# Kernel optimization log

Measured on AMD Instinct MI355X. Metric: run time of the kernel, lower is better.

The kernel has to match this reference:

```python
import jax, jax.numpy as jnp
import numpy as np
import math

B, N, D = 128, 50, 256      # batch, segments per piece, cross-attn feature dim
H_CA = 8                    # cross-attention heads
FP, H_AP = 64, 8            # pooling feature dim / heads
S = N * N                   # flattened similarity length (<= 2560 pos-enc cap)
TEMP = 1.0
LN_EPS = 1e-5


def _ln(x, g, b):
    mu = jnp.mean(x, -1, keepdims=True)
    var = jnp.mean((x - mu) ** 2, -1, keepdims=True)
    return (x - mu) * jax.lax.rsqrt(var + LN_EPS) * g + b


def setup_inputs() -> dict:
    key = jax.random.key(0)
    ks = jax.random.split(key, 32)
    w = lambda i, shp, s=0.02: jax.random.normal(ks[i], shp, jnp.float32) * s
    z = lambda shp: jnp.zeros(shp, jnp.float32)
    o = lambda shp: jnp.ones(shp, jnp.float32)
    return {
        "features1": jax.random.normal(ks[0], (B, N, D), jnp.float32),
        "features2": jax.random.normal(ks[1], (B, N, D), jnp.float32),
        # CrossAttention (weights stored (in,out) so x @ W + b)
        "ca_wq": w(2, (D, D)), "ca_bq": z((D,)),
        "ca_wk": w(3, (D, D)), "ca_bk": z((D,)),
        "ca_wv": w(4, (D, D)), "ca_bv": z((D,)),
        "ca_wo": w(5, (D, D)), "ca_bo": z((D,)),
        "ca_ln1_g": o((D,)), "ca_ln1_b": z((D,)),
        "ca_ln2_g": o((D,)), "ca_ln2_b": z((D,)),
        "ca_w1": w(6, (D, 2 * D)), "ca_b1": z((2 * D,)),
        "ca_w2": w(7, (2 * D, D)), "ca_b2": z((D,)),
        # LearnableMetricSimilarity
        "ms_metric": jnp.eye(D, dtype=jnp.float32),
        "ms_wt": w(8, (D, D)), "ms_bt": z((D,)),
        # AttentionPooling
        "ap_wq": w(9, (1, FP)), "ap_bq": z((FP,)),
        "ap_wk": w(10, (1, FP)), "ap_bk": z((FP,)),
        "ap_wv": w(11, (1, FP)), "ap_bv": z((FP,)),
        "ap_pos": w(12, (1, 2560, FP), 0.02),
        "ap_wo": w(13, (FP, FP)), "ap_bo": z((FP,)),
        "ap_ln_g": o((FP,)), "ap_ln_b": z((FP,)),
    }


def reference(features1, features2,
              ca_wq, ca_bq, ca_wk, ca_bk, ca_wv, ca_bv, ca_wo, ca_bo,
              ca_ln1_g, ca_ln1_b, ca_ln2_g, ca_ln2_b,
              ca_w1, ca_b1, ca_w2, ca_b2,
              ms_metric, ms_wt, ms_bt,
              ap_wq, ap_bq, ap_wk, ap_bk, ap_wv, ap_bv,
              ap_pos, ap_wo, ap_bo, ap_ln_g, ap_ln_b):
    hd = D // H_CA

    def attend(fx, fy):
        q = (fx @ ca_wq + ca_bq).reshape(B, N, H_CA, hd)
        k = (fy @ ca_wk + ca_bk).reshape(B, N, H_CA, hd)
        v = (fy @ ca_wv + ca_bv).reshape(B, N, H_CA, hd)
        # Faithful to original: tensors stay (B,N,H,hd), so matmul with
        # k.transpose(-2,-1) yields per-position head-vs-head attention (B,N,H,H).
        scores = jnp.einsum('bnhd,bngd->bnhg', q, k) / math.sqrt(hd)
        wts = jax.nn.softmax(scores, axis=-1)  # dropout is identity (eval)
        att = jnp.einsum('bnhg,bngd->bnhd', wts, v).reshape(B, N, D)
        x = _ln(fx + att @ ca_wo + ca_bo, ca_ln1_g, ca_ln1_b)
        ffn = jax.nn.relu(x @ ca_w1 + ca_b1) @ ca_w2 + ca_b2
        return _ln(x + ffn, ca_ln2_g, ca_ln2_b)

    e1 = attend(features1, features2)
    e2 = attend(features2, features1)

    # Learnable metric similarity: Mahalanobis distance via quadratic expansion
    # d_ij = t1_i M t1_i + t2_j M t2_j - 2 t1_i M t2_j  (M symmetrized)
    t1 = e1 @ ms_wt + ms_bt
    t2 = e2 @ ms_wt + ms_bt
    M = (ms_metric + ms_metric.T) * 0.5
    t1M = t1 @ M
    t2M = t2 @ M
    q1 = jnp.sum(t1M * t1, axis=-1)                    # (B,N)
    q2 = jnp.sum(t2M * t2, axis=-1)                    # (B,N)
    cross = jnp.einsum('bnd,bmd->bnm', t1M, t2)        # (B,N,N)
    dist = q1[:, :, None] + q2[:, None, :] - 2.0 * cross
    sim = jnp.exp(jnp.clip(-dist / TEMP, -10.0, 10.0))  # (B,N,N)

    # Attention pooling over flattened similarity matrix
    flat = sim.reshape(B, S, 1)
    pos = ap_pos[:, :S, :]
    hdp = FP // H_AP
    q = (flat @ ap_wq + ap_bq + pos).reshape(B, S, H_AP, hdp)
    k = (flat @ ap_wk + ap_bk + pos).reshape(B, S, H_AP, hdp)
    v = (flat @ ap_wv + ap_bv).reshape(B, S, H_AP, hdp)
    scores = jnp.einsum('bshd,bsgd->bshg', q, k) / math.sqrt(hdp)  # (B,S,H,H)
    wts = jax.nn.softmax(scores, axis=-1)
    att = jnp.einsum('bshg,bsgd->bshd', wts, v).reshape(B, S, FP)
    pooled = jnp.mean(att, axis=1) @ ap_wo + ap_bo     # (B,FP)
    return _ln(pooled, ap_ln_g, ap_ln_b)
```

## Files before the change

kernel.cpp:

```cpp
#include <hip/hip_runtime.h>
#include <cstddef>
#include <cstdint>


namespace esn {

constexpr int kB   = 128;
constexpr int kN   = 50;
constexpr int kR   = kB * kN;
constexpr int kR2  = 2 * kR;
constexpr int kS   = kN * kN;
constexpr int kChunks = 79;

typedef __attribute__((ext_vector_type(8))) short short8;
typedef __attribute__((ext_vector_type(4))) float f32x4;

__device__ inline ushort f2bf_rn(float v) {
  uint32_t u = __float_as_uint(v);
  uint32_t r = (u + 0x7fffu + ((u >> 16) & 1u)) >> 16;
  return (ushort)r;
}
__device__ inline float bf2f(ushort b) {
  return __uint_as_float(((uint32_t)b) << 16);
}
__device__ inline void split2(float v, ushort& h, ushort& l) {
  h = f2bf_rn(v);
  l = f2bf_rn(v - bf2f(h));
}

__device__ __forceinline__ void gld16(const ushort* g, ushort* l) {
  __builtin_amdgcn_global_load_lds(
      (const __attribute__((address_space(1))) void*)g,
      (__attribute__((address_space(3))) void*)l,
      16, 0, 0);
}

template<bool RELU, bool WF32, bool WSPLIT>
__global__ __launch_bounds__(256)
void gemm_mfma_kernel(const ushort* __restrict__ Ah, const ushort* __restrict__ Al, int lda,
                      const ushort* __restrict__ Bh, const ushort* __restrict__ Bl, int ldb,
                      const float* __restrict__ bias,
                      float* __restrict__ C, int ldc,
                      ushort* __restrict__ Ch, ushort* __restrict__ Cl,
                      int K)
{
  __shared__ __align__(16) ushort sAh[128 * 32];
  __shared__ __align__(16) ushort sAl[128 * 32];
  __shared__ __align__(16) ushort sBh[128 * 32];
  __shared__ __align__(16) ushort sBl[128 * 32];

  const int tid  = threadIdx.x;
  const int lane = tid & 63;
  const int wave = tid >> 6;
  const int wm   = wave >> 1, wn = wave & 1;
  const int bm   = blockIdx.x * 128, bn = blockIdx.y * 128;

  const int lrow  = lane >> 2;
  const int lslot = lane & 3;

  f32x4 acc[4][4] = {};

  const int nK = K >> 5;
  for (int kt = 0; kt < nK; kt++) {
    const int kk = kt << 5;
#pragma unroll
    for (int i = 0; i < 2; i++) {
      const int grp  = wave * 32 + i * 16;
      const int row  = grp + lrow;
      const int c    = lslot ^ ((row >> 1) & 3);
      const size_t aoff = (size_t)(bm + row) * lda + kk + c * 8;
      const size_t boff = (size_t)(bn + row) * ldb + kk + c * 8;
      gld16(Ah + aoff, sAh + grp * 32);
      gld16(Al + aoff, sAl + grp * 32);
      gld16(Bh + boff, sBh + grp * 32);
      gld16(Bl + boff, sBl + grp * 32);
    }
    __syncthreads();

    const int r16 = lane & 15, kq = lane >> 4;
    short8 afh[4], afl[4], bfh[4], bfl[4];
#pragma unroll
    for (int f = 0; f < 4; f++) {
      int arow = wm * 64 + f * 16 + r16;
      int sa = kq ^ ((arow >> 1) & 3);
      afh[f] = *(const short8*)(sAh + arow * 32 + sa * 8);
      afl[f] = *(const short8*)(sAl + arow * 32 + sa * 8);
      int brow = wn * 64 + f * 16 + r16;
      int sb = kq ^ ((brow >> 1) & 3);
      bfh[f] = *(const short8*)(sBh + brow * 32 + sb * 8);
      bfl[f] = *(const short8*)(sBl + brow * 32 + sb * 8);
    }
#pragma unroll
    for (int mf = 0; mf < 4; mf++)
#pragma unroll
      for (int nf = 0; nf < 4; nf++) {
        acc[mf][nf] = __builtin_amdgcn_mfma_f32_16x16x32_bf16(afh[mf], bfh[nf], acc[mf][nf], 0, 0, 0);
        acc[mf][nf] = __builtin_amdgcn_mfma_f32_16x16x32_bf16(afh[mf], bfl[nf], acc[mf][nf], 0, 0, 0);
        acc[mf][nf] = __builtin_amdgcn_mfma_f32_16x16x32_bf16(afl[mf], bfh[nf], acc[mf][nf], 0, 0, 0);
      }
    __syncthreads();
  }

  const int r16 = lane & 15, rq = lane >> 4;
#pragma unroll
  for (int nf = 0; nf < 4; nf++) {
    int col = bn + wn * 64 + nf * 16 + r16;
    float bv = bias ? bias[col] : 0.0f;
#pragma unroll
    for (int mf = 0; mf < 4; mf++) {
      int rowb = bm + wm * 64 + mf * 16 + rq * 4;
#pragma unroll
      for (int r = 0; r < 4; r++) {
        float v = acc[mf][nf][r] + bv;
        if (RELU) v = fmaxf(v, 0.0f);
        size_t off = (size_t)(rowb + r) * ldc + col;
        if (WF32) C[off] = v;
        if (WSPLIT) {
          ushort h, l; split2(v, h, l);
          Ch[off] = h; Cl[off] = l;
        }
      }
    }
  }
}

__global__ void prep_w_kernel(const float* __restrict__ wq, const float* __restrict__ wk,
                              const float* __restrict__ wv, const float* __restrict__ bq,
                              const float* __restrict__ bk, const float* __restrict__ bv,
                              const float* __restrict__ wo, const float* __restrict__ w1,
                              const float* __restrict__ w2, const float* __restrict__ wt,
                              const float* __restrict__ msm,
                              ushort* __restrict__ qkvh, ushort* __restrict__ qkvl,
                              ushort* __restrict__ woh,  ushort* __restrict__ wol,
                              ushort* __restrict__ w1h,  ushort* __restrict__ w1l,
                              ushort* __restrict__ w2h,  ushort* __restrict__ w2l,
                              ushort* __restrict__ wth,  ushort* __restrict__ wtl,
                              ushort* __restrict__ msh,  ushort* __restrict__ msl,
                              float* __restrict__ bqkv)
{
  int idx = blockIdx.x * 256 + threadIdx.x;
  if (idx < 768)
    bqkv[idx] = idx < 256 ? bq[idx] : idx < 512 ? bk[idx - 256] : bv[idx - 512];
  float v; ushort *oh, *ol; int off;
  if (idx < 196608) {
    int n = idx >> 8, k = idx & 255;
    v = n < 256 ? wq[k * 256 + n] : n < 512 ? wk[k * 256 + n - 256] : wv[k * 256 + n - 512];
    oh = qkvh; ol = qkvl; off = idx;
  } else if (idx < 262144) {
    int i = idx - 196608; int n = i >> 8, k = i & 255;
    v = wo[k * 256 + n]; oh = woh; ol = wol; off = i;
  } else if (idx < 393216) {
    int i = idx - 262144; int n = i >> 8, k = i & 255;
    v = w1[k * 512 + n]; oh = w1h; ol = w1l; off = i;
  } else if (idx < 524288) {
    int i = idx - 393216; int n = i >> 9, k = i & 511;
    v = w2[k * 256 + n]; oh = w2h; ol = w2l; off = i;
  } else if (idx < 589824) {
    int i = idx - 524288; int n = i >> 8, k = i & 255;
    v = wt[k * 256 + n]; oh = wth; ol = wtl; off = i;
  } else if (idx < 655360) {
    int i = idx - 589824; int n = i >> 8, k = i & 255;
    v = 0.5f * (msm[k * 256 + n] + msm[n * 256 + k]); oh = msh; ol = msl; off = i;
  } else return;
  ushort h, l; split2(v, h, l);
  oh[off] = h; ol[off] = l;
}

__global__ void split_f_kernel(const float* __restrict__ f1, const float* __restrict__ f2,
                               ushort* __restrict__ Fh, ushort* __restrict__ Fl)
{
  int idx = (blockIdx.x * 256 + threadIdx.x) * 4;
  const float* src = idx < kR * 256 ? f1 + idx : f2 + (idx - kR * 256);
  float4 v = *(const float4*)src;
  ushort h, l;
  split2(v.x, h, l); Fh[idx + 0] = h; Fl[idx + 0] = l;
  split2(v.y, h, l); Fh[idx + 1] = h; Fl[idx + 1] = l;
  split2(v.z, h, l); Fh[idx + 2] = h; Fl[idx + 2] = l;
  split2(v.w, h, l); Fh[idx + 3] = h; Fl[idx + 3] = l;
}

__global__ __launch_bounds__(256)
void ca_attn_kernel(const float* __restrict__ P, ushort* __restrict__ Ah,
                    ushort* __restrict__ Al)
{
  const int rib  = threadIdx.x >> 6;
  const int row  = blockIdx.x * 4 + rib;
  const int lane = threadIdx.x & 63;
  const int partner = (row < kR) ? row + kR : row - kR;
  const float* q = P + (size_t)row * 768;
  const float* k = P + (size_t)partner * 768 + 256;
  const float* v = P + (size_t)partner * 768 + 512;
  const int h = lane >> 3, g = lane & 7;

  float s = 0.0f;
#pragma unroll
  for (int i = 0; i < 8; i++) {
    float4 qa = *(const float4*)(q + h * 32 + i * 4);
    float4 ka = *(const float4*)(k + g * 32 + i * 4);
    s = fmaf(qa.x, ka.x, s); s = fmaf(qa.y, ka.y, s);
    s = fmaf(qa.z, ka.z, s); s = fmaf(qa.w, ka.w, s);
  }
  s *= 0.17677669529663687f;

  float mx = s;
#pragma unroll
  for (int d = 1; d < 8; d <<= 1) mx = fmaxf(mx, __shfl_xor(mx, d));
  float e = expf(s - mx);
  float se = e;
#pragma unroll
  for (int d = 1; d < 8; d <<= 1) se += __shfl_xor(se, d);
  float w = e / se;

  __shared__ float lds_w[4][64];
  lds_w[rib][lane] = w;
  __syncthreads();

  const int dc = lane & 7;
  float o[4] = {};
#pragma unroll
  for (int gg = 0; gg < 8; gg++) {
    float wg = lds_w[rib][h * 8 + gg];
    float4 va = *(const float4*)(v + gg * 32 + dc * 4);
    o[0] = fmaf(wg, va.x, o[0]); o[1] = fmaf(wg, va.y, o[1]);
    o[2] = fmaf(wg, va.z, o[2]); o[3] = fmaf(wg, va.w, o[3]);
  }
  size_t base = (size_t)row * 256 + h * 32 + dc * 4;
#pragma unroll
  for (int j = 0; j < 4; j++) {
    ushort hh, ll; split2(o[j], hh, ll);
    Ah[base + j] = hh; Al[base + j] = ll;
  }
}

template<bool WF32>
__global__ __launch_bounds__(256)
void ln_res_kernel(const float* __restrict__ Y, const float* __restrict__ R1,
                   const float* __restrict__ R2, const float* __restrict__ g,
                   const float* __restrict__ b, float* __restrict__ X,
                   ushort* __restrict__ Xh, ushort* __restrict__ Xl)
{
  const int row  = blockIdx.x * 4 + (threadIdx.x >> 6);
  const int lane = threadIdx.x & 63;
  const float* res = (row < kR) ? (R1 + (size_t)row * 256)
                                : (R2 + (size_t)(row - kR) * 256);
  float4 y4 = *(const float4*)(Y + (size_t)row * 256 + lane * 4);
  float4 r4 = *(const float4*)(res + lane * 4);
  float v[4] = {y4.x + r4.x, y4.y + r4.y, y4.z + r4.z, y4.w + r4.w};

  float ssum = v[0] + v[1] + v[2] + v[3];
#pragma unroll
  for (int d = 1; d < 64; d <<= 1) ssum += __shfl_xor(ssum, d);
  float mu = ssum * (1.0f / 256.0f);
  float qq = 0.0f;
#pragma unroll
  for (int j = 0; j < 4; j++) { float dv = v[j] - mu; qq = fmaf(dv, dv, qq); }
#pragma unroll
  for (int d = 1; d < 64; d <<= 1) qq += __shfl_xor(qq, d);
  float rstd = rsqrtf(qq * (1.0f / 256.0f) + 1e-5f);

  float4 g4 = *(const float4*)(g + lane * 4);
  float4 b4 = *(const float4*)(b + lane * 4);
  float o[4];
  o[0] = (v[0] - mu) * rstd * g4.x + b4.x;
  o[1] = (v[1] - mu) * rstd * g4.y + b4.y;
  o[2] = (v[2] - mu) * rstd * g4.z + b4.z;
  o[3] = (v[3] - mu) * rstd * g4.w + b4.w;
  size_t base = (size_t)row * 256 + lane * 4;
  if (WF32) *(float4*)(X + base) = *(float4*)o;
#pragma unroll
  for (int j = 0; j < 4; j++) {
    ushort hh, ll; split2(o[j], hh, ll);
    Xh[base + j] = hh; Xl[base + j] = ll;
  }
}

__global__ __launch_bounds__(256)
void qdot_kernel(const float* __restrict__ T, const float* __restrict__ TM,
                 float* __restrict__ QD)
{
  const int row  = blockIdx.x * 4 + (threadIdx.x >> 6);
  const int lane = threadIdx.x & 63;
  float4 a = *(const float4*)(T  + (size_t)row * 256 + lane * 4);
  float4 b = *(const float4*)(TM + (size_t)row * 256 + lane * 4);
  float s = a.x * b.x + a.y * b.y + a.z * b.z + a.w * b.w;
#pragma unroll
  for (int d = 1; d < 64; d <<= 1) s += __shfl_xor(s, d);
  if (lane == 0) QD[row] = s;
}

__global__ __launch_bounds__(256)
void cross_kernel(const float* __restrict__ T1M, const float* __restrict__ T2,
                  float* __restrict__ CP)
{
  const int b  = blockIdx.x >> 1;
  const int kh = blockIdx.x & 1;
  __shared__ float sA[128][64];
  __shared__ float sB[128][64];
  const int tid = threadIdx.x;
#pragma unroll
  for (int i = 0; i < 8; i++) {
    int slot = tid + i * 256;
    int n  = slot >> 5;
    int k4 = (slot & 31) * 4;
    float4 a = make_float4(0.f, 0.f, 0.f, 0.f), c = a;
    if (n < 50) {
      a = *(const float4*)(T1M + ((size_t)b * 50 + n) * 256 + kh * 128 + k4);
      c = *(const float4*)(T2  + ((size_t)kR + b * 50 + n) * 256 + kh * 128 + k4);
    }
    sA[k4 + 0][n] = a.x; sA[k4 + 1][n] = a.y; sA[k4 + 2][n] = a.z; sA[k4 + 3][n] = a.w;
    sB[k4 + 0][n] = c.x; sB[k4 + 1][n] = c.y; sB[k4 + 2][n] = c.z; sB[k4 + 3][n] = c.w;
  }
  __syncthreads();
  const int tn = tid & 15, tm = tid >> 4;
  const int n0 = tn * 4, m0 = tm * 4;
  float acc[4][4] = {};
  for (int k = 0; k < 128; k++) {
    float4 a4 = *(const float4*)(&sA[k][n0]);
    float4 b4 = *(const float4*)(&sB[k][m0]);
    float a[4] = {a4.x, a4.y, a4.z, a4.w};
    float c[4] = {b4.x, b4.y, b4.z, b4.w};
#pragma unroll
    for (int i = 0; i < 4; i++)
#pragma unroll
      for (int j = 0; j < 4; j++)
        acc[i][j] = fmaf(a[i], c[j], acc[i][j]);
  }
#pragma unroll
  for (int i = 0; i < 4; i++) {
    float* cp = CP + (((size_t)b * 2 + kh) * 64 + n0 + i) * 64 + m0;
    *(float4*)cp = *(float4*)(&acc[i][0]);
  }
}

__global__ void sim_kernel(const float* __restrict__ CP, const float* __restrict__ QD,
                           float* __restrict__ SIM)
{
  int idx = blockIdx.x * 256 + threadIdx.x;
  if (idx >= kB * kS) return;
  int b = idx / kS, s = idx % kS;
  int n = s / kN, m = s % kN;
  float c = CP[(((size_t)b * 2 + 0) * 64 + n) * 64 + m]
          + CP[(((size_t)b * 2 + 1) * 64 + n) * 64 + m];
  float dist = QD[b * kN + n] + QD[kR + b * kN + m] - 2.0f * c;
  float z = -dist;
  z = fminf(fmaxf(z, -10.0f), 10.0f);
  SIM[idx] = expf(z);
}

__global__ __launch_bounds__(256)
void ap_kernel(const float* __restrict__ SIM, const float* __restrict__ pos,
               const float* __restrict__ wq, const float* __restrict__ bq,
               const float* __restrict__ wk, const float* __restrict__ bk,
               const float* __restrict__ wv, const float* __restrict__ bv,
               float* __restrict__ PP)
{
  const int b  = blockIdx.x / kChunks;
  const int ch = blockIdx.x % kChunks;
  const int sl = threadIdx.x >> 3;
  const int h  = threadIdx.x & 7;
  const int s  = ch * 32 + sl;
  const bool valid = (s < kS);

  __shared__ float sk[32][64];
  __shared__ float sv[32][64];
  __shared__ float satt[32][64];

  float f = valid ? SIM[(size_t)b * kS + s] : 0.0f;
  const float* pp = pos + (valid ? (size_t)s * 64 : 0) + h * 8;

  float qv[8];
#pragma unroll
  for (int d = 0; d < 8; d++) {
    int c = h * 8 + d;
    float pd = pp[d];
    qv[d] = fmaf(f, wq[c], bq[c] + pd);
    sk[sl][c] = fmaf(f, wk[c], bk[c] + pd);
    sv[sl][c] = fmaf(f, wv[c], bv[c]);
  }
  __syncthreads();

  float sc[8];
#pragma unroll
  for (int g = 0; g < 8; g++) {
    const float* kr = &sk[sl][g * 8];
    float a = 0.0f;
#pragma unroll
    for (int d = 0; d < 8; d++) a = fmaf(qv[d], kr[d], a);
    sc[g] = a * 0.35355339059327373f;
  }
  float mx = sc[0];
#pragma unroll
  for (int g = 1; g < 8; g++) mx = fmaxf(mx, sc[g]);
  float se = 0.0f;
#pragma unroll
  for (int g = 0; g < 8; g++) { sc[g] = expf(sc[g] - mx); se += sc[g]; }
  float inv = 1.0f / se;

  float av[8] = {};
#pragma unroll
  for (int g = 0; g < 8; g++) {
    float wg = sc[g] * inv;
    const float* vr = &sv[sl][g * 8];
#pragma unroll
    for (int d = 0; d < 8; d++) av[d] = fmaf(wg, vr[d], av[d]);
  }
  if (!valid) {
#pragma unroll
    for (int d = 0; d < 8; d++) av[d] = 0.0f;
  }
#pragma unroll
  for (int d = 0; d < 8; d++) satt[sl][h * 8 + d] = av[d];
  __syncthreads();

  for (int st = 16; st >= 1; st >>= 1) {
    if (sl < st) {
#pragma unroll
      for (int d = 0; d < 8; d++)
        satt[sl][h * 8 + d] += satt[sl + st][h * 8 + d];
    }
    __syncthreads();
  }
  if (sl == 0) {
#pragma unroll
    for (int d = 0; d < 8; d++)
      PP[((size_t)b * kChunks + ch) * 64 + h * 8 + d] = satt[0][h * 8 + d];
  }
}

__global__ __launch_bounds__(64)
void final_kernel(const float* __restrict__ PP, const float* __restrict__ wo,
                  const float* __restrict__ bo, const float* __restrict__ lg,
                  const float* __restrict__ lb, float* __restrict__ out)
{
  const int b = blockIdx.x, j = threadIdx.x;
  double acc = 0.0;
  for (int c = 0; c < kChunks; c++)
    acc += (double)PP[((size_t)b * kChunks + c) * 64 + j];
  double pooled = acc / 2500.0;
  __shared__ double sp[64];
  sp[j] = pooled;
  __syncthreads();
  double o = (double)bo[j];
  for (int d = 0; d < 64; d++) o += sp[d] * (double)wo[d * 64 + j];
  double ssum = o;
#pragma unroll
  for (int d2 = 1; d2 < 64; d2 <<= 1) ssum += __shfl_xor(ssum, d2);
  double mu = ssum / 64.0;
  double dv = o - mu;
  double qq = dv * dv;
#pragma unroll
  for (int d2 = 1; d2 < 64; d2 <<= 1) qq += __shfl_xor(qq, d2);
  double var = qq / 64.0;
  double r = 1.0 / sqrt(var + 1e-5);
  out[(size_t)b * 64 + j] = (float)(dv * r * (double)lg[j] + (double)lb[j]);
}

}

extern "C" void kernel_launch(void* const* d_in, const int* in_sizes, int n_in,
                              void* d_out, int out_size, void* d_ws, size_t ws_size,
                              hipStream_t stream)
{
  using namespace esn;
  const float* f1      = (const float*)d_in[0];
  const float* f2      = (const float*)d_in[1];
  const float* ca_wq   = (const float*)d_in[2];
  const float* ca_bq   = (const float*)d_in[3];
  const float* ca_wk   = (const float*)d_in[4];
  const float* ca_bk   = (const float*)d_in[5];
  const float* ca_wv   = (const float*)d_in[6];
  const float* ca_bv   = (const float*)d_in[7];
  const float* ca_wo   = (const float*)d_in[8];
  const float* ca_bo   = (const float*)d_in[9];
  const float* ln1_g   = (const float*)d_in[10];
  const float* ln1_b   = (const float*)d_in[11];
  const float* ln2_g   = (const float*)d_in[12];
  const float* ln2_b   = (const float*)d_in[13];
  const float* ca_w1   = (const float*)d_in[14];
  const float* ca_b1   = (const float*)d_in[15];
  const float* ca_w2   = (const float*)d_in[16];
  const float* ca_b2   = (const float*)d_in[17];
  const float* ms_met  = (const float*)d_in[18];
  const float* ms_wt   = (const float*)d_in[19];
  const float* ms_bt   = (const float*)d_in[20];
  const float* ap_wq   = (const float*)d_in[21];
  const float* ap_bq   = (const float*)d_in[22];
  const float* ap_wk   = (const float*)d_in[23];
  const float* ap_bk   = (const float*)d_in[24];
  const float* ap_wv   = (const float*)d_in[25];
  const float* ap_bv   = (const float*)d_in[26];
  const float* ap_pos  = (const float*)d_in[27];
  const float* ap_wo   = (const float*)d_in[28];
  const float* ap_bo   = (const float*)d_in[29];
  const float* ap_ln_g = (const float*)d_in[30];
  const float* ap_ln_b = (const float*)d_in[31];

  float* ws = (float*)d_ws;
  float*  P    = ws;
  ushort* Hh   = (ushort*)(ws);
  ushort* Hl   = (ushort*)(ws + 3276800);
  float*  TM   = ws;
  ushort* Th   = (ushort*)(ws + 3276800);
  ushort* Tl   = (ushort*)(ws + 4915200);
  float*  Tt   = ws + 6553600;
  ushort* S1h  = (ushort*)(ws + 9830400);
  ushort* S1l  = (ushort*)(ws + 11468800);
  float*  X    = ws + 13107200;
  float*  Y    = ws + 16384000;
  float*  CP   = ws + 16384000;
  float*  SIM  = ws + 17432576;
  float*  PP   = ws + 17752576;
  float*  QD   = ws + 19660800;
  ushort* Wqh  = (ushort*)(ws + 19673600);
  ushort* Wql  = (ushort*)(ws + 19771904);
  ushort* Woh  = (ushort*)(ws + 19870208);
  ushort* Wol  = (ushort*)(ws + 19902976);
  ushort* W1h  = (ushort*)(ws + 19935744);
  ushort* W1l  = (ushort*)(ws + 20001280);
  ushort* W2h  = (ushort*)(ws + 20066816);
  ushort* W2l  = (ushort*)(ws + 20132352);
  ushort* Wth  = (ushort*)(ws + 20197888);
  ushort* Wtl  = (ushort*)(ws + 20230656);
  ushort* Msh  = (ushort*)(ws + 20263424);
  ushort* Msl  = (ushort*)(ws + 20296192);
  float*  BQKV = ws + 20328960;

  prep_w_kernel<<<2560, 256, 0, stream>>>(ca_wq, ca_wk, ca_wv, ca_bq, ca_bk, ca_bv,
                                          ca_wo, ca_w1, ca_w2, ms_wt, ms_met,
                                          Wqh, Wql, Woh, Wol, W1h, W1l, W2h, W2l,
                                          Wth, Wtl, Msh, Msl, BQKV);
  split_f_kernel<<<3200, 256, 0, stream>>>(f1, f2, S1h, S1l);
  gemm_mfma_kernel<false, true, false><<<dim3(100, 6), 256, 0, stream>>>(
      S1h, S1l, 256, Wqh, Wql, 256, BQKV, P, 768, nullptr, nullptr, 256);
  ca_attn_kernel<<<kR2 / 4, 256, 0, stream>>>(P, S1h, S1l);
  gemm_mfma_kernel<false, true, false><<<dim3(100, 2), 256, 0, stream>>>(
      S1h, S1l, 256, Woh, Wol, 256, ca_bo, Y, 256, nullptr, nullptr, 256);
  ln_res_kernel<true><<<kR2 / 4, 256, 0, stream>>>(Y, f1, f2, ln1_g, ln1_b, X, S1h, S1l);
  gemm_mfma_kernel<true, false, true><<<dim3(100, 4), 256, 0, stream>>>(
      S1h, S1l, 256, W1h, W1l, 256, ca_b1, nullptr, 512, Hh, Hl, 256);
  gemm_mfma_kernel<false, true, false><<<dim3(100, 2), 256, 0, stream>>>(
      Hh, Hl, 512, W2h, W2l, 512, ca_b2, Y, 256, nullptr, nullptr, 512);
  ln_res_kernel<false><<<kR2 / 4, 256, 0, stream>>>(Y, X, X + (size_t)kR * 256,
                                                    ln2_g, ln2_b, nullptr, S1h, S1l);
  gemm_mfma_kernel<false, true, true><<<dim3(100, 2), 256, 0, stream>>>(
      S1h, S1l, 256, Wth, Wtl, 256, ms_bt, Tt, 256, Th, Tl, 256);
  gemm_mfma_kernel<false, true, false><<<dim3(100, 2), 256, 0, stream>>>(
      Th, Tl, 256, Msh, Msl, 256, nullptr, TM, 256, nullptr, nullptr, 256);
  qdot_kernel<<<kR2 / 4, 256, 0, stream>>>(Tt, TM, QD);
  cross_kernel<<<kB * 2, 256, 0, stream>>>(TM, Tt, CP);
  sim_kernel<<<(kB * kS + 255) / 256, 256, 0, stream>>>(CP, QD, SIM);
  ap_kernel<<<kB * kChunks, 256, 0, stream>>>(SIM, ap_pos, ap_wq, ap_bq, ap_wk, ap_bk,
                                              ap_wv, ap_bv, PP);
  final_kernel<<<kB, 64, 0, stream>>>(PP, ap_wo, ap_bo, ap_ln_g, ap_ln_b, (float*)d_out);
}
```

Before: 259.0 us.

## Algebraically factor attention pooling into precomputed score tables and deferred V projection

The attention-pooling scores are rewritten as a quadratic in the scalar similarity value: f²·(wq·wk) + f·T1 + T0, where T1 and T0 come from tables precomputed from the positional encodings and weights. A new kernel builds those tables independently of the input features. The main kernel no longer forms q/k/v per position. It accumulates softmax weight sums and f-weighted sums per head pair, and the final kernel applies the value projection (wv, bv) afterwards. This removes most per-position arithmetic and shared-memory traffic, at the cost of an extra table read per position, fast exp, and a different float summation order.

```diff
diff --git a/kernel.cpp b/kernel.cpp
--- a/kernel.cpp
+++ b/kernel.cpp
@@ -10,7 +10,6 @@
 constexpr int kR   = kB * kN;
 constexpr int kR2  = 2 * kR;
 constexpr int kS   = kN * kN;
-constexpr int kChunks = 79;
 
 typedef __attribute__((ext_vector_type(8))) short short8;
 typedef __attribute__((ext_vector_type(4))) float f32x4;
@@ -348,100 +347,99 @@
 }
 
 __global__ __launch_bounds__(256)
-void ap_kernel(const float* __restrict__ SIM, const float* __restrict__ pos,
-               const float* __restrict__ wq, const float* __restrict__ bq,
-               const float* __restrict__ wk, const float* __restrict__ bk,
-               const float* __restrict__ wv, const float* __restrict__ bv,
-               float* __restrict__ PP)
-{
-  const int b  = blockIdx.x / kChunks;
-  const int ch = blockIdx.x % kChunks;
-  const int sl = threadIdx.x >> 3;
-  const int h  = threadIdx.x & 7;
-  const int s  = ch * 32 + sl;
-  const bool valid = (s < kS);
-
-  __shared__ float sk[32][64];
-  __shared__ float sv[32][64];
-  __shared__ float satt[32][64];
-
-  float f = valid ? SIM[(size_t)b * kS + s] : 0.0f;
-  const float* pp = pos + (valid ? (size_t)s * 64 : 0) + h * 8;
-
-  float qv[8];
+void ap_tables_kernel(const float* __restrict__ pos,
+                      const float* __restrict__ wq, const float* __restrict__ bq,
+                      const float* __restrict__ wk, const float* __restrict__ bk,
+                      float2* __restrict__ TT)
+{
+  int idx = blockIdx.x * 256 + threadIdx.x;
+  if (idx >= kS * 64) return;
+  int s = idx >> 6, lane = idx & 63;
+  int h = lane >> 3, g = lane & 7;
+  float t1 = 0.f, t0 = 0.f;
 #pragma unroll
   for (int d = 0; d < 8; d++) {
-    int c = h * 8 + d;
-    float pd = pp[d];
-    qv[d] = fmaf(f, wq[c], bq[c] + pd);
-    sk[sl][c] = fmaf(f, wk[c], bk[c] + pd);
-    sv[sl][c] = fmaf(f, wv[c], bv[c]);
-  }
-  __syncthreads();
-
-  float sc[8];
-#pragma unroll
-  for (int g = 0; g < 8; g++) {
-    const float* kr = &sk[sl][g * 8];
-    float a = 0.0f;
-#pragma unroll
-    for (int d = 0; d < 8; d++) a = fmaf(qv[d], kr[d], a);
-    sc[g] = a * 0.35355339059327373f;
-  }
-  float mx = sc[0];
-#pragma unroll
-  for (int g = 1; g < 8; g++) mx = fmaxf(mx, sc[g]);
-  float se = 0.0f;
-#pragma unroll
-  for (int g = 0; g < 8; g++) { sc[g] = expf(sc[g] - mx); se += sc[g]; }
-  float inv = 1.0f / se;
-
-  float av[8] = {};
-#pragma unroll
-  for (int g = 0; g < 8; g++) {
-    float wg = sc[g] * inv;
-    const float* vr = &sv[sl][g * 8];
-#pragma unroll
-    for (int d = 0; d < 8; d++) av[d] = fmaf(wg, vr[d], av[d]);
-  }
-  if (!valid) {
-#pragma unroll
-    for (int d = 0; d < 8; d++) av[d] = 0.0f;
-  }
-#pragma unroll
-  for (int d = 0; d < 8; d++) satt[sl][h * 8 + d] = av[d];
-  __syncthreads();
-
-  for (int st = 16; st >= 1; st >>= 1) {
-    if (sl < st) {
-#pragma unroll
-      for (int d = 0; d < 8; d++)
-        satt[sl][h * 8 + d] += satt[sl + st][h * 8 + d];
-    }
-    __syncthreads();
-  }
-  if (sl == 0) {
-#pragma unroll
-    for (int d = 0; d < 8; d++)
-      PP[((size_t)b * kChunks + ch) * 64 + h * 8 + d] = satt[0][h * 8 + d];
-  }
+    float a  = wq[h * 8 + d];
+    float c  = bq[h * 8 + d] + pos[s * 64 + h * 8 + d];
+    float bb = wk[g * 8 + d];
+    float e  = bk[g * 8 + d] + pos[s * 64 + g * 8 + d];
+    t1 = fmaf(a, e, t1);
+    t1 = fmaf(c, bb, t1);
+    t0 = fmaf(c, e, t0);
+  }
+  TT[idx] = make_float2(t1, t0);
+}
+
+__global__ __launch_bounds__(256)
+void ap_kernel(const float* __restrict__ SIM, const float2* __restrict__ TT,
+               const float* __restrict__ wq, const float* __restrict__ wk,
+               float* __restrict__ GP)
+{
+  const int b    = blockIdx.x;
+  const int sb   = blockIdx.y;
+  const int wave = threadIdx.x >> 6, lane = threadIdx.x & 63;
+  const int strip = sb * 4 + wave;
+  const int h = lane >> 3, g = lane & 7;
+
+  float A2 = 0.f;
+#pragma unroll
+  for (int d = 0; d < 8; d++) A2 = fmaf(wq[h * 8 + d], wk[g * 8 + d], A2);
+  const float inv8 = 0.35355339059327373f;
+
+  float G0 = 0.f, G1 = 0.f;
+  const int s0 = strip * 79;
+  const int s1 = (s0 + 79 < kS) ? s0 + 79 : kS;
+  for (int s = s0; s < s1; s++) {
+    float f = SIM[(size_t)b * kS + s];
+    float2 t = TT[s * 64 + lane];
+    float x = fmaf(f * f, A2, fmaf(f, t.x, t.y)) * inv8;
+    float mx = x;
+    mx = fmaxf(mx, __shfl_xor(mx, 1));
+    mx = fmaxf(mx, __shfl_xor(mx, 2));
+    mx = fmaxf(mx, __shfl_xor(mx, 4));
+    float e = __expf(x - mx);
+    float se = e;
+    se += __shfl_xor(se, 1);
+    se += __shfl_xor(se, 2);
+    se += __shfl_xor(se, 4);
+    float w = e / se;
+    G0 += w;
+    G1 = fmaf(w, f, G1);
+  }
+  float* gp = GP + (((size_t)b * 32 + strip) * 2) * 64;
+  gp[lane]      = G1;
+  gp[64 + lane] = G0;
 }
 
 __global__ __launch_bounds__(64)
-void final_kernel(const float* __restrict__ PP, const float* __restrict__ wo,
+void final_kernel(const float* __restrict__ GP, const float* __restrict__ wv,
+                  const float* __restrict__ bv, const float* __restrict__ wo,
                   const float* __restrict__ bo, const float* __restrict__ lg,
                   const float* __restrict__ lb, float* __restrict__ out)
 {
   const int b = blockIdx.x, j = threadIdx.x;
-  double acc = 0.0;
-  for (int c = 0; c < kChunks; c++)
-    acc += (double)PP[((size_t)b * kChunks + c) * 64 + j];
-  double pooled = acc / 2500.0;
+  float G1 = 0.f, G0 = 0.f;
+  for (int st = 0; st < 32; st++) {
+    const float* gp = GP + (((size_t)b * 32 + st) * 2) * 64;
+    G1 += gp[j];
+    G0 += gp[64 + j];
+  }
+  __shared__ float sg1[64], sg0[64];
+  sg1[j] = G1; sg0[j] = G0;
+  __syncthreads();
+  const int h = j >> 3, d = j & 7;
+  float acc = 0.f;
+#pragma unroll
+  for (int g = 0; g < 8; g++) {
+    acc = fmaf(sg1[h * 8 + g], wv[g * 8 + d], acc);
+    acc = fmaf(sg0[h * 8 + g], bv[g * 8 + d], acc);
+  }
+  double pooled = (double)acc / 2500.0;
   __shared__ double sp[64];
   sp[j] = pooled;
   __syncthreads();
   double o = (double)bo[j];
-  for (int d = 0; d < 64; d++) o += sp[d] * (double)wo[d * 64 + j];
+  for (int dd = 0; dd < 64; dd++) o += sp[dd] * (double)wo[dd * 64 + j];
   double ssum = o;
 #pragma unroll
   for (int d2 = 1; d2 < 64; d2 <<= 1) ssum += __shfl_xor(ssum, d2);
@@ -509,7 +507,8 @@
   float*  Y    = ws + 16384000;
   float*  CP   = ws + 16384000;
   float*  SIM  = ws + 17432576;
-  float*  PP   = ws + 17752576;
+  float*  GP   = ws + 17752576;
+  float2* TT   = (float2*)(ws + 18399744);
   float*  QD   = ws + 19660800;
   ushort* Wqh  = (ushort*)(ws + 19673600);
   ushort* Wql  = (ushort*)(ws + 19771904);
@@ -530,6 +529,7 @@
                                           Wqh, Wql, Woh, Wol, W1h, W1l, W2h, W2l,
                                           Wth, Wtl, Msh, Msl, BQKV);
   split_f_kernel<<<3200, 256, 0, stream>>>(f1, f2, S1h, S1l);
+  ap_tables_kernel<<<625, 256, 0, stream>>>(ap_pos, ap_wq, ap_bq, ap_wk, ap_bk, TT);
   gemm_mfma_kernel<false, true, false><<<dim3(100, 6), 256, 0, stream>>>(
       S1h, S1l, 256, Wqh, Wql, 256, BQKV, P, 768, nullptr, nullptr, 256);
   ca_attn_kernel<<<kR2 / 4, 256, 0, stream>>>(P, S1h, S1l);
@@ -549,7 +549,7 @@
   qdot_kernel<<<kR2 / 4, 256, 0, stream>>>(Tt, TM, QD);
   cross_kernel<<<kB * 2, 256, 0, stream>>>(TM, Tt, CP);
   sim_kernel<<<(kB * kS + 255) / 256, 256, 0, stream>>>(CP, QD, SIM);
-  ap_kernel<<<kB * kChunks, 256, 0, stream>>>(SIM, ap_pos, ap_wq, ap_bq, ap_wk, ap_bk,
-                                              ap_wv, ap_bv, PP);
-  final_kernel<<<kB, 64, 0, stream>>>(PP, ap_wo, ap_bo, ap_ln_g, ap_ln_b, (float*)d_out);
-}
+  ap_kernel<<<dim3(kB, 8), 256, 0, stream>>>(SIM, TT, ap_wq, ap_wk, GP);
+  final_kernel<<<kB, 64, 0, stream>>>(GP, ap_wv, ap_bv, ap_wo, ap_bo,
+                                      ap_ln_g, ap_ln_b, (float*)d_out);
+}
```

New measurement: 253.5 us. 1.02x faster.
